# Kernel tuning notes

Measured on AMD Instinct MI355X. Metric: run time of the kernel, lower is better.

The kernel has to match this reference:

```python
import jax, jax.numpy as jnp
import numpy as np

D_MODEL = 1024
D_STATE = 16
EXPAND = 2
D_INNER = EXPAND * D_MODEL
DT_RANK = 64  # ceil(1024/16)
D_CONV = 4


def setup_inputs() -> dict:
    key = jax.random.key(0)
    ks = jax.random.split(key, 8)
    s = 0.02
    x = jax.random.normal(ks[0], (2, 2048, D_MODEL), dtype=jnp.float32)
    W_in = jax.random.normal(ks[1], (D_MODEL, 2 * D_INNER), dtype=jnp.float32) * s
    W_conv = jax.random.normal(ks[2], (D_CONV, D_INNER), dtype=jnp.float32) * s  # depthwise taps
    b_conv = jnp.zeros((D_INNER,), dtype=jnp.float32)
    W_xproj = jax.random.normal(ks[3], (D_INNER, DT_RANK + 2 * D_STATE), dtype=jnp.float32) * s
    W_dt = jax.random.normal(ks[4], (DT_RANK, D_INNER), dtype=jnp.float32) * s
    b_dt = jnp.zeros((D_INNER,), dtype=jnp.float32)
    A_log = jnp.broadcast_to(jnp.log(jnp.arange(1, D_STATE + 1, dtype=jnp.float32)), (D_INNER, D_STATE))
    D = jnp.ones((D_INNER,), dtype=jnp.float32)
    W_out = jax.random.normal(ks[5], (D_INNER, D_MODEL), dtype=jnp.float32) * s
    return {"x": x, "W_in": W_in, "W_conv": W_conv, "b_conv": b_conv,
            "W_xproj": W_xproj, "W_dt": W_dt, "b_dt": b_dt,
            "A_log": A_log, "D": D, "W_out": W_out}


def _silu(v):
    return v * jax.nn.sigmoid(v)


def reference(x, W_in, W_conv, b_conv, W_xproj, W_dt, b_dt, A_log, D, W_out):
    B_, L, _ = x.shape
    xz = x @ W_in                     # [B, L, 2*d_inner]
    x_in, z = jnp.split(xz, 2, axis=-1)
    # causal depthwise conv1d (torch padding=d_conv-1 then slice to seq_len)
    pad = D_CONV - 1
    x_pad = jnp.pad(x_in, ((0, 0), (pad, 0), (0, 0)))
    x_conv = b_conv
    x_conv = sum(x_pad[:, k:k + L, :] * W_conv[k] for k in range(D_CONV)) + b_conv
    x_in = _silu(x_conv)              # [B, L, d_inner]
    dbc = x_in @ W_xproj
    dt = jax.nn.softplus(dbc[..., :DT_RANK] @ W_dt + b_dt)   # [B, L, d_inner]
    Bm = dbc[..., DT_RANK:DT_RANK + D_STATE]                  # [B, L, d_state]
    Cm = dbc[..., DT_RANK + D_STATE:]                          # [B, L, d_state]
    A = -jnp.exp(A_log)                                        # [d_inner, d_state]

    def step(state, inp):
        x_t, dt_t, B_t, C_t = inp   # [B,d_inner], [B,d_inner], [B,d_state], [B,d_state]
        dA = jnp.exp(jnp.clip(dt_t[:, :, None] * A[None], -10.0, 10.0))
        dB = dt_t[:, :, None] * B_t[:, None, :]
        state = jnp.clip(state * dA + x_t[:, :, None] * dB, -10.0, 10.0)
        y_t = jnp.einsum('bdn,bn->bd', state, C_t) + D * x_t
        return state, y_t

    tm = lambda a: jnp.swapaxes(a, 0, 1)  # time-major
    state0 = jnp.zeros((B_, D_INNER, D_STATE), dtype=x.dtype)
    _, ys = jax.lax.scan(step, state0, (tm(x_in), tm(dt), tm(Bm), tm(Cm)))
    y = jnp.swapaxes(ys, 0, 1)            # [B, L, d_inner]
    y = y * _silu(z)
    return y @ W_out                       # [B, L, d_model]
```

## Files before the change

### kernel.cpp

```cpp
#include <hip/hip_runtime.h>
#include <math.h>

#define D_MODEL 1024
#define D_INNER 2048
#define D_STATE 16
#define DT_RANK 64
#define LSEQ 2048
#define NBATCH 2
#define M_TOT (NBATCH * LSEQ)
#define DBC_STRIDE 128
#define CH 64
#define NCH (LSEQ / CH)
#define KSPL 8
#define OKSPL 2

typedef unsigned short ushort_t;
typedef unsigned int uint_t;
typedef __attribute__((ext_vector_type(8))) short bf16x8;
typedef __attribute__((ext_vector_type(4))) float f32x4;

__device__ __forceinline__ ushort_t f2bf_rne(float f) {
    uint_t u = __float_as_uint(f);
    u += 0x7fffu + ((u >> 16) & 1u);
    return (ushort_t)(u >> 16);
}
__device__ __forceinline__ float bf2f(ushort_t h) {
    return __uint_as_float(((uint_t)h) << 16);
}
__device__ __forceinline__ float fexp2(float x) {
#if __has_builtin(__builtin_amdgcn_exp2f)
    return __builtin_amdgcn_exp2f(x);
#else
    return exp2f(x);
#endif
}
__device__ __forceinline__ float frcp(float x) {
#if __has_builtin(__builtin_amdgcn_rcpf)
    return __builtin_amdgcn_rcpf(x);
#else
    return 1.f / x;
#endif
}
__device__ __forceinline__ float clip10(float x) {
#if __has_builtin(__builtin_amdgcn_fmed3f)
    return __builtin_amdgcn_fmed3f(x, -10.f, 10.f);
#else
    return fminf(fmaxf(x, -10.f), 10.f);
#endif
}

#define LOG2E 1.44269504f
#define NLOG2E10 -14.4269504f

#define BAR()   __builtin_amdgcn_s_barrier()
#define LGKM0() asm volatile("s_waitcnt lgkmcnt(0)" ::: "memory")
#define GLDS(SRC, DST)                                                         \
    __builtin_amdgcn_global_load_lds(                                          \
        (const __attribute__((address_space(1))) void*)(SRC),                  \
        (__attribute__((address_space(3))) void*)(DST), 16, 0, 0)

#define LDFRAG_B(SRC)                                                          \
    _Pragma("unroll")                                                          \
    for (int nf = 0; nf < 4; ++nf)                                             \
        fB[nf] = *reinterpret_cast<const bf16x8*>(                             \
            &(SRC)[(bRow + nf * 16 + fm) * 32 + swz * 8]);

#define LDFRAG_A(SRC, MOFF)                                                    \
    _Pragma("unroll")                                                          \
    for (int mf = 0; mf < 4; ++mf)                                             \
        fA[mf] = *reinterpret_cast<const bf16x8*>(                             \
            &(SRC)[(aRow + (MOFF + mf) * 16 + fm) * 32 + swz * 8]);

#define MFMA_QUAD(MOFF)                                                        \
    __builtin_amdgcn_s_setprio(1);                                             \
    _Pragma("unroll")                                                          \
    for (int mf = 0; mf < 4; ++mf)                                             \
        _Pragma("unroll")                                                      \
        for (int nf = 0; nf < 4; ++nf)                                         \
            acc[MOFF + mf][nf] = __builtin_amdgcn_mfma_f32_16x16x32_bf16(      \
                fA[mf], fB[nf], acc[MOFF + mf][nf], 0, 0, 0);                  \
    __builtin_amdgcn_s_setprio(0);

#define KIN 1024
#define KTI (KIN / 64)

__global__ __launch_bounds__(512, 2) void gemm256_inproj(
    const ushort_t* __restrict__ Ah, const ushort_t* __restrict__ BTh,
    float* __restrict__ C, float* __restrict__ AUX)
{
    __shared__ __align__(1024) ushort_t smem[65536];
    const int tid  = threadIdx.x;
    const int lane = tid & 63;
    const int w    = tid >> 6;
    const int wm   = w >> 2;
    const int wn   = w & 3;
    const int fm   = lane & 15, fk = lane >> 4;
    const int swz  = fk ^ ((fm >> 1) & 3);
    const int aRow = wm * 128;
    const int bRow = wn * 64;
    const int m0   = blockIdx.y * 256;
    const int n0   = blockIdx.x * 256;
    const int rbase = w * 16 + (lane >> 2);
    const int ssw   = ((lane & 3) ^ ((lane >> 3) & 3)) * 8;

    f32x4 acc[8][4] = {};

    auto stage = [&](const ushort_t* __restrict__ g, int grow0, int kcol,
                     int regUS) {
        #pragma unroll
        for (int q = 0; q < 2; ++q) {
            const ushort_t* src =
                g + (size_t)(grow0 + q * 128 + rbase) * KIN + kcol + ssw;
            GLDS(src, smem + regUS + q * 4096 + w * 512);
        }
    };

    stage(Ah,  m0, 0,  0);
    stage(BTh, n0, 0,  32768);
    stage(Ah,  m0, 32, 8192);
    stage(BTh, n0, 32, 32768 + 8192);
    stage(Ah,  m0, 64, 16384);
    stage(BTh, n0, 64, 32768 + 16384);
    asm volatile("s_waitcnt vmcnt(8)" ::: "memory");
    BAR();

    bf16x8 fA[4], fB[4];

    for (int t = 0; t < KTI - 1; ++t) {
        const int bf = t & 1, bn = bf ^ 1;
        const ushort_t* A0 = smem + (bf * 2 + 0) * 8192;
        const ushort_t* A1 = smem + (bf * 2 + 1) * 8192;
        const ushort_t* B0 = smem + 32768 + (bf * 2 + 0) * 8192;
        const ushort_t* B1 = smem + 32768 + (bf * 2 + 1) * 8192;
        const int kc1 = (t + 1) * 64, kc2 = (t + 2) * 64;
        const bool st2 = (t + 2 < KTI);

        LDFRAG_B(B0);
        LDFRAG_A(A0, 0);
        stage(Ah, m0, kc1 + 32, (bn * 2 + 1) * 8192);
        BAR(); LGKM0();
        MFMA_QUAD(0);
        BAR();

        LDFRAG_A(A0, 4);
        stage(BTh, n0, kc1 + 32, 32768 + (bn * 2 + 1) * 8192);
        BAR(); LGKM0();
        MFMA_QUAD(4);
        asm volatile("s_waitcnt vmcnt(8)" ::: "memory");
        BAR();
        __builtin_amdgcn_sched_barrier(0);

        LDFRAG_B(B1);
        LDFRAG_A(A1, 0);
        if (st2) stage(Ah, m0, kc2, (bf * 2 + 0) * 8192);
        BAR(); LGKM0();
        MFMA_QUAD(0);
        BAR();

        LDFRAG_A(A1, 4);
        if (st2) stage(BTh, n0, kc2, 32768 + (bf * 2 + 0) * 8192);
        BAR(); LGKM0();
        MFMA_QUAD(4);
        if (t == KTI - 2) { asm volatile("s_waitcnt vmcnt(4)" ::: "memory"); }
        else              { asm volatile("s_waitcnt vmcnt(6)" ::: "memory"); }
        BAR();
        __builtin_amdgcn_sched_barrier(0);
    }

    {
        const int bf = (KTI - 1) & 1;
        const ushort_t* A0 = smem + (bf * 2 + 0) * 8192;
        const ushort_t* A1 = smem + (bf * 2 + 1) * 8192;
        const ushort_t* B0 = smem + 32768 + (bf * 2 + 0) * 8192;
        const ushort_t* B1 = smem + 32768 + (bf * 2 + 1) * 8192;

        LDFRAG_B(B0);
        LDFRAG_A(A0, 0);
        BAR(); LGKM0();
        MFMA_QUAD(0);
        BAR();

        LDFRAG_A(A0, 4);
        BAR(); LGKM0();
        MFMA_QUAD(4);
        asm volatile("s_waitcnt vmcnt(0)" ::: "memory");
        BAR();

        LDFRAG_B(B1);
        LDFRAG_A(A1, 0);
        BAR(); LGKM0();
        MFMA_QUAD(0);
        BAR();

        LDFRAG_A(A1, 4);
        BAR(); LGKM0();
        MFMA_QUAD(4);
    }

    float* dst = (n0 < D_INNER) ? C : AUX;
    const int csub = (n0 < D_INNER) ? 0 : D_INNER;
    #pragma unroll
    for (int mf = 0; mf < 8; ++mf) {
        int row0 = m0 + aRow + mf * 16 + fk * 4;
        #pragma unroll
        for (int nf = 0; nf < 4; ++nf) {
            int col = n0 + bRow + nf * 16 + fm - csub;
            #pragma unroll
            for (int r = 0; r < 4; ++r)
                dst[(size_t)(row0 + r) * D_INNER + col] = acc[mf][nf][r];
        }
    }
}

#define KOUT 2048
#define NTOUT 16

__global__ __launch_bounds__(512, 2) void gemm256_outproj(
    const ushort_t* __restrict__ Ah, const ushort_t* __restrict__ BTh,
    const ushort_t* __restrict__ BTl, float* __restrict__ P)
{
    __shared__ __align__(1024) ushort_t smem[65536];
    const int tid  = threadIdx.x;
    const int lane = tid & 63;
    const int w    = tid >> 6;
    const int wm   = w & 3;
    const int wn   = w >> 2;
    const int fm   = lane & 15, fk = lane >> 4;
    const int swz  = fk ^ ((fm >> 1) & 3);
    const int aRow = wm * 64;
    const int bRow = wn * 64;
    const int ks   = blockIdx.x >> 3;
    const int n0   = (blockIdx.x & 7) * 128;
    const int m0   = blockIdx.y * 256;
    const int kb   = ks * (KOUT / OKSPL);
    const int rbase = w * 16 + (lane >> 2);
    const int ssw   = ((lane & 3) ^ ((lane >> 3) & 3)) * 8;

    f32x4 acc[4][4] = {};

    auto stageA = [&](int t, int kh) {
        const int kcol = kb + t * 64 + kh * 32;
        const int reg = ((t & 1) * 2 + kh) * 8192;
        #pragma unroll
        for (int q = 0; q < 2; ++q) {
            const ushort_t* src =
                Ah + (size_t)(m0 + q * 128 + rbase) * KOUT + kcol + ssw;
            GLDS(src, smem + reg + q * 4096 + w * 512);
        }
    };
    auto stageB = [&](const ushort_t* __restrict__ B, int base, int t, int kh) {
        const int kcol = kb + t * 64 + kh * 32;
        const int reg = base + ((t & 1) * 2 + kh) * 4096;
        const ushort_t* src = B + (size_t)(n0 + rbase) * KOUT + kcol + ssw;
        GLDS(src, smem + reg + w * 512);
    };

    stageA(0, 0);
    stageA(0, 1);
    stageB(BTh, 32768, 0, 0);
    stageB(BTh, 32768, 0, 1);
    stageB(BTl, 49152, 0, 0);
    stageB(BTl, 49152, 0, 1);
    asm volatile("s_waitcnt vmcnt(3)" ::: "memory");
    BAR();

    bf16x8 fA[4], fB[4];

    for (int t = 0; t < NTOUT - 1; ++t) {
        const int bf = t & 1;
        const ushort_t* A0  = smem + (bf * 2 + 0) * 8192;
        const ushort_t* A1  = smem + (bf * 2 + 1) * 8192;
        const ushort_t* Bh0 = smem + 32768 + (bf * 2 + 0) * 4096;
        const ushort_t* Bh1 = smem + 32768 + (bf * 2 + 1) * 4096;
        const ushort_t* Bl0 = smem + 49152 + (bf * 2 + 0) * 4096;
        const ushort_t* Bl1 = smem + 49152 + (bf * 2 + 1) * 4096;

        LDFRAG_B(Bh0);
        LDFRAG_A(A0, 0);
        stageA(t + 1, 0);
        BAR(); LGKM0();
        MFMA_QUAD(0);
        asm volatile("s_waitcnt vmcnt(3)" ::: "memory");
        BAR();
        __builtin_amdgcn_sched_barrier(0);

        LDFRAG_B(Bl0);
        stageA(t + 1, 1);
        BAR(); LGKM0();
        MFMA_QUAD(0);
        BAR();

        LDFRAG_B(Bh1);
        LDFRAG_A(A1, 0);
        stageB(BTh, 32768, t + 1, 0);
        stageB(BTh, 32768, t + 1, 1);
        BAR(); LGKM0();
        MFMA_QUAD(0);
        asm volatile("s_waitcnt vmcnt(6)" ::: "memory");
        BAR();
        __builtin_amdgcn_sched_barrier(0);

        LDFRAG_B(Bl1);
        stageB(BTl, 49152, t + 1, 0);
        stageB(BTl, 49152, t + 1, 1);
        BAR(); LGKM0();
        MFMA_QUAD(0);
        asm volatile("s_waitcnt vmcnt(3)" ::: "memory");
        BAR();
        __builtin_amdgcn_sched_barrier(0);
    }

    {
        const int bf = (NTOUT - 1) & 1;
        const ushort_t* A0  = smem + (bf * 2 + 0) * 8192;
        const ushort_t* A1  = smem + (bf * 2 + 1) * 8192;
        const ushort_t* Bh0 = smem + 32768 + (bf * 2 + 0) * 4096;
        const ushort_t* Bh1 = smem + 32768 + (bf * 2 + 1) * 4096;
        const ushort_t* Bl0 = smem + 49152 + (bf * 2 + 0) * 4096;
        const ushort_t* Bl1 = smem + 49152 + (bf * 2 + 1) * 4096;

        LDFRAG_B(Bh0);
        LDFRAG_A(A0, 0);
        BAR(); LGKM0();
        MFMA_QUAD(0);
        asm volatile("s_waitcnt vmcnt(1)" ::: "memory");
        BAR();

        LDFRAG_B(Bl0);
        BAR(); LGKM0();
        MFMA_QUAD(0);
        BAR();

        LDFRAG_B(Bh1);
        LDFRAG_A(A1, 0);
        BAR(); LGKM0();
        MFMA_QUAD(0);
        asm volatile("s_waitcnt vmcnt(0)" ::: "memory");
        BAR();

        LDFRAG_B(Bl1);
        BAR(); LGKM0();
        MFMA_QUAD(0);
    }

    float* Pq = P + (size_t)ks * M_TOT * D_MODEL;
    #pragma unroll
    for (int mf = 0; mf < 4; ++mf) {
        int row0 = m0 + aRow + mf * 16 + fk * 4;
        #pragma unroll
        for (int nf = 0; nf < 4; ++nf) {
            int col = n0 + bRow + nf * 16 + fm;
            #pragma unroll
            for (int r = 0; r < 4; ++r)
                Pq[(size_t)(row0 + r) * D_MODEL + col] = acc[mf][nf][r];
        }
    }
}

template <int MODE, int TERMS>
__global__ __launch_bounds__(256) void gemm_bf16s(
    const ushort_t* __restrict__ Ah, const ushort_t* __restrict__ Al,
    const ushort_t* __restrict__ BTh, const ushort_t* __restrict__ BTl,
    float* __restrict__ C, float* __restrict__ AUX, int M, int N, int K)
{
    __shared__ __align__(16) ushort_t smem[4 * 128 * 32];
    ushort_t* sAh = smem;
    ushort_t* sAl = smem + 4096;
    ushort_t* sBh = smem + 8192;
    ushort_t* sBl = smem + 12288;
    const int tid = threadIdx.x;
    const int lane = tid & 63;
    const int m0 = blockIdx.y * 128;
    int ks = 0, nblk = blockIdx.x;
    if (MODE == 3) { ks = blockIdx.x; nblk = 0; }
    const int n0 = nblk * 128;
    const int wave = tid >> 6;
    const int mw = (wave & 1) * 64, nw = (wave >> 1) * 64;
    const int fm = lane & 15, fk = lane >> 4;
    const int swz = fk ^ ((fm >> 1) & 3);

    f32x4 acc[4][4] = {};

    const int r_st0 = tid >> 2, cp0 = tid & 3;
    const int r_st1 = (256 + tid) >> 2, cp1 = tid & 3;
    const int cl0 = cp0 ^ ((r_st0 >> 1) & 3);
    const int cl1 = cp1 ^ ((r_st1 >> 1) & 3);
    const int ldsb0 = (tid & ~63) * 16;
    const int ldsb1 = (256 + (tid & ~63)) * 16;

    const int kbeg = (MODE == 3) ? ks * (K / KSPL) : 0;
    const int kend = (MODE == 3) ? kbeg + K / KSPL : K;

    for (int k0 = kbeg; k0 < kend; k0 += 32) {
        __syncthreads();
        {
            size_t ga0 = (size_t)(m0 + r_st0) * K + k0 + cl0 * 8;
            size_t ga1 = (size_t)(m0 + r_st1) * K + k0 + cl1 * 8;
            size_t gb0 = (size_t)(n0 + r_st0) * K + k0 + cl0 * 8;
            size_t gb1 = (size_t)(n0 + r_st1) * K + k0 + cl1 * 8;
            GLDS(Ah + ga0, (char*)sAh + ldsb0);
            GLDS(Ah + ga1, (char*)sAh + ldsb1);
            if (TERMS >= 3) {
                GLDS(Al + ga0, (char*)sAl + ldsb0);
                GLDS(Al + ga1, (char*)sAl + ldsb1);
            }
            GLDS(BTh + gb0, (char*)sBh + ldsb0);
            GLDS(BTh + gb1, (char*)sBh + ldsb1);
            if (TERMS >= 2) {
                GLDS(BTl + gb0, (char*)sBl + ldsb0);
                GLDS(BTl + gb1, (char*)sBl + ldsb1);
            }
        }
        __syncthreads();

        bf16x8 fAh[4], fAl[4], fBh[4], fBl[4];
        #pragma unroll
        for (int t = 0; t < 4; ++t) {
            int ra = (mw + t * 16 + fm) * 32 + swz * 8;
            int rb = (nw + t * 16 + fm) * 32 + swz * 8;
            fAh[t] = *reinterpret_cast<const bf16x8*>(&sAh[ra]);
            if (TERMS >= 3) fAl[t] = *reinterpret_cast<const bf16x8*>(&sAl[ra]);
            fBh[t] = *reinterpret_cast<const bf16x8*>(&sBh[rb]);
            if (TERMS >= 2) fBl[t] = *reinterpret_cast<const bf16x8*>(&sBl[rb]);
        }
        #pragma unroll
        for (int i = 0; i < 4; ++i)
            #pragma unroll
            for (int j = 0; j < 4; ++j) {
                acc[i][j] = __builtin_amdgcn_mfma_f32_16x16x32_bf16(fAh[i], fBh[j], acc[i][j], 0, 0, 0);
                if (TERMS >= 3)
                    acc[i][j] = __builtin_amdgcn_mfma_f32_16x16x32_bf16(fAl[i], fBh[j], acc[i][j], 0, 0, 0);
                if (TERMS >= 2)
                    acc[i][j] = __builtin_amdgcn_mfma_f32_16x16x32_bf16(fAh[i], fBl[j], acc[i][j], 0, 0, 0);
            }
    }

    float* Cq = (MODE == 3) ? C + (size_t)ks * M * N : C;
    #pragma unroll
    for (int i = 0; i < 4; ++i) {
        int row0 = m0 + mw + i * 16 + fk * 4;
        #pragma unroll
        for (int j = 0; j < 4; ++j) {
            int col = n0 + nw + j * 16 + fm;
            if (MODE == 5) {
                const float* bias = (const float*)AUX;
                float bc_ = bias[col];
                #pragma unroll
                for (int r = 0; r < 4; ++r) {
                    float t = acc[i][j][r] + bc_;
                    C[(size_t)(row0 + r) * N + col] =
                        fmaxf(t, 0.f) + log1pf(__expf(-fabsf(t)));
                }
            } else {
                #pragma unroll
                for (int r = 0; r < 4; ++r)
                    Cq[(size_t)(row0 + r) * N + col] = acc[i][j][r];
            }
        }
    }
}

__global__ __launch_bounds__(256) void xproj_red_k(
    const float* __restrict__ dbcp, float* __restrict__ dbc,
    ushort_t* __restrict__ dbch)
{
    int g = blockIdx.x * 256 + threadIdx.x;
    int m = g >> 7, c = g & 127;
    float s = 0.f;
    #pragma unroll
    for (int ks = 0; ks < KSPL; ++ks)
        s += dbcp[(size_t)ks * M_TOT * DBC_STRIDE + g];
    dbc[g] = s;
    if (c < 64)
        dbch[(size_t)m * 64 + c] = f2bf_rne(s);
}

__global__ __launch_bounds__(256) void outred_k(
    const float* __restrict__ p, float* __restrict__ out)
{
    int i4 = (blockIdx.x * 256 + threadIdx.x) * 4;
    f32x4 a = *reinterpret_cast<const f32x4*>(p + i4);
    f32x4 b = *reinterpret_cast<const f32x4*>(p + (size_t)M_TOT * D_MODEL + i4);
    *reinterpret_cast<f32x4*>(out + i4) = a + b;
}

__global__ __launch_bounds__(256) void cast_h_k(
    const float* __restrict__ X, ushort_t* __restrict__ Xh)
{
    int i4 = (blockIdx.x * 256 + threadIdx.x) * 4;
    float4 v = *reinterpret_cast<const float4*>(X + i4);
    ushort2 a = make_ushort2(f2bf_rne(v.x), f2bf_rne(v.y));
    ushort2 b = make_ushort2(f2bf_rne(v.z), f2bf_rne(v.w));
    *reinterpret_cast<ushort2*>(Xh + i4)     = a;
    *reinterpret_cast<ushort2*>(Xh + i4 + 2) = b;
}

__global__ __launch_bounds__(256) void transpose_cast_k(
    const float* __restrict__ W, ushort_t* __restrict__ Th, ushort_t* __restrict__ Tl,
    int K, int N)
{
    __shared__ float tile[32][33];
    int n0 = blockIdx.x * 32, k0 = blockIdx.y * 32;
    int tx = threadIdx.x & 31, ty = threadIdx.x >> 5;
    #pragma unroll
    for (int i = 0; i < 32; i += 8)
        tile[ty + i][tx] = W[(size_t)(k0 + ty + i) * N + n0 + tx];
    __syncthreads();
    #pragma unroll
    for (int i = 0; i < 32; i += 8) {
        float v = tile[tx][ty + i];
        ushort_t h = f2bf_rne(v);
        ushort_t l = f2bf_rne(v - bf2f(h));
        size_t o = (size_t)(n0 + ty + i) * K + k0 + tx;
        Th[o] = h; Tl[o] = l;
    }
}

__global__ __launch_bounds__(256) void transpose_cast_pad_k(
    const float* __restrict__ W, ushort_t* __restrict__ Th, int K, int N)
{
    __shared__ float tile[32][33];
    int n0 = blockIdx.x * 32, k0 = blockIdx.y * 32;
    int tx = threadIdx.x & 31, ty = threadIdx.x >> 5;
    #pragma unroll
    for (int i = 0; i < 32; i += 8)
        tile[ty + i][tx] = (n0 + tx < N) ? W[(size_t)(k0 + ty + i) * N + n0 + tx] : 0.f;
    __syncthreads();
    #pragma unroll
    for (int i = 0; i < 32; i += 8) {
        float v = tile[tx][ty + i];
        size_t o = (size_t)(n0 + ty + i) * K + k0 + tx;
        Th[o] = f2bf_rne(v);
    }
}

__global__ __launch_bounds__(256) void conv_silu_k(
    const float* __restrict__ xbuf, const float* __restrict__ Wc,
    const float* __restrict__ bc, ushort_t* __restrict__ xinh,
    float* __restrict__ xf)
{
    __shared__ float tile[67][64];
    const int c0 = blockIdx.x * 64;
    const int m0 = blockIdx.y * 64;
    const int bstart = m0 & ~(LSEQ - 1);
    const int tid = threadIdx.x;

    for (int e = tid; e < 67 * 64; e += 256) {
        int r = e >> 6, c = e & 63;
        int g = m0 - 3 + r;
        tile[r][c] = (g >= bstart) ? xbuf[(size_t)g * D_INNER + c0 + c] : 0.f;
    }
    __syncthreads();

    const int c_l = tid & 63, mg = tid >> 6;
    const int c = c0 + c_l;
    const float w0 = Wc[c], w1 = Wc[D_INNER + c];
    const float w2 = Wc[2 * D_INNER + c], w3 = Wc[3 * D_INNER + c];
    const float bb = bc[c];
    #pragma unroll
    for (int mi = 0; mi < 16; ++mi) {
        int r = mg * 16 + mi;
        float acc = bb + tile[r][c_l] * w0 + tile[r + 1][c_l] * w1
                       + tile[r + 2][c_l] * w2 + tile[r + 3][c_l] * w3;
        float sv = acc / (1.f + __expf(-acc));
        xinh[(size_t)(m0 + r) * D_INNER + c] = f2bf_rne(sv);
        xf[(size_t)(m0 + r) * D_INNER + c] = sv;
    }
}

__global__ __launch_bounds__(256) void scan_sum_k4(
    const float* __restrict__ dtf, const float* __restrict__ xf,
    const float* __restrict__ dbc, const float* __restrict__ A_log,
    float* __restrict__ asumb, float* __restrict__ sendb)
{
    __shared__ float sdt[2][8][256];
    __shared__ float sx[2][8][256];
    __shared__ float sB[64][16];
    const int tid = threadIdx.x;
    const int lane = tid & 63;
    const int w = tid >> 6;
    const int c0 = blockIdx.x << 8;
    const int ck = blockIdx.y;
    const int b  = blockIdx.z;
    const size_t mbase = (size_t)b * LSEQ + (size_t)ck * CH;
    const int d = c0 + tid;

    auto stageG = [&](int G, int bf) {
        #pragma unroll
        for (int p = 0; p < 2; ++p) {
            const int r = w + p * 4;
            const size_t g = (mbase + G * 8 + r) * D_INNER + c0 + lane * 4;
            GLDS(dtf + g, &sdt[bf][r][0]);
            GLDS(xf + g,  &sx[bf][r][0]);
        }
    };

    {
        const int rbc = w * 16 + (lane >> 2);
        GLDS(dbc + (mbase + rbc) * DBC_STRIDE + 64 + (lane & 3) * 4,
             &sB[w * 16][0]);
    }
    stageG(0, 0);
    stageG(1, 1);

    float AdnL2[16];
    #pragma unroll
    for (int n = 0; n < 16; ++n)
        AdnL2[n] = -__expf(A_log[d * D_STATE + n]) * LOG2E;

    float s[16] = {};
    float asum[16] = {};

    asm volatile("s_waitcnt vmcnt(4)" ::: "memory");
    BAR();

    for (int G = 0; G < 8; ++G) {
        const int bf = G & 1;
        #pragma unroll
        for (int t = 0; t < 8; ++t) {
            const int rr = G * 8 + t;
            const float dv = sdt[bf][t][tid];
            const float xv = sx[bf][t][tid];
            const float p  = dv * xv;
            #pragma unroll
            for (int n = 0; n < 16; ++n) {
                float a = fmaxf(dv * AdnL2[n], NLOG2E10);
                asum[n] += a;
                float e = fexp2(a);
                s[n] = clip10(fmaf(s[n], e, p * sB[rr][n]));
            }
        }
        BAR();
        if (G + 2 < 8) {
            stageG(G + 2, bf);
            asm volatile("s_waitcnt vmcnt(4)" ::: "memory");
        } else if (G == 6) {
            asm volatile("s_waitcnt vmcnt(0)" ::: "memory");
        }
        BAR();
        __builtin_amdgcn_sched_barrier(0);
    }

    #pragma unroll
    for (int n = 0; n < 16; ++n) {
        size_t o = (((size_t)(b * NCH + ck) * 16) + n) * D_INNER + d;
        asumb[o] = asum[n];
        sendb[o] = s[n];
    }
}

__global__ __launch_bounds__(256) void scan_fix_k2(
    const float* __restrict__ asumb, const float* __restrict__ sendb,
    float* __restrict__ sinb)
{
    int g = blockIdx.x * 256 + threadIdx.x;
    int d = g & (D_INNER - 1);
    int n = (g >> 11) & 15;
    int b = g >> 15;
    float s = 0.f;
    for (int ck = 0; ck < NCH; ++ck) {
        size_t idx = (((size_t)(b * NCH + ck) * 16) + n) * D_INNER + d;
        sinb[idx] = s;
        s = clip10(fmaf(s, fexp2(asumb[idx]), sendb[idx]));
    }
}

__global__ __launch_bounds__(256) void scan_apply_k4(
    const float* __restrict__ dtf, const float* __restrict__ xf,
    const float* __restrict__ dbc, const float* __restrict__ zf,
    const float* __restrict__ sinb, const float* __restrict__ A_log,
    const float* __restrict__ Dv, ushort_t* __restrict__ Yh)
{
    __shared__ float sdt[2][8][256];
    __shared__ float sx[2][8][256];
    __shared__ float sz[2][8][256];
    __shared__ float sBC[64][32];
    const int tid = threadIdx.x;
    const int lane = tid & 63;
    const int w = tid >> 6;
    const int c0 = blockIdx.x << 8;
    const int ck = blockIdx.y;
    const int b  = blockIdx.z;
    const size_t mbase = (size_t)b * LSEQ + (size_t)ck * CH;
    const int d = c0 + tid;

    auto stageG = [&](int G, int bf) {
        #pragma unroll
        for (int p = 0; p < 2; ++p) {
            const int r = w + p * 4;
            const size_t g = (mbase + G * 8 + r) * D_INNER + c0 + lane * 4;
            GLDS(dtf + g, &sdt[bf][r][0]);
            GLDS(xf + g,  &sx[bf][r][0]);
            GLDS(zf + g,  &sz[bf][r][0]);
        }
    };

    #pragma unroll
    for (int p = 0; p < 2; ++p) {
        const int rbc = w * 16 + p * 8 + (lane >> 3);
        GLDS(dbc + (mbase + rbc) * DBC_STRIDE + 64 + (lane & 7) * 4,
             &sBC[w * 16 + p * 8][0]);
    }
    stageG(0, 0);
    stageG(1, 1);

    float AdnL2[16];
    #pragma unroll
    for (int n = 0; n < 16; ++n)
        AdnL2[n] = -__expf(A_log[d * D_STATE + n]) * LOG2E;
    const float Dd = Dv[d];

    float s[16];
    #pragma unroll
    for (int n = 0; n < 16; ++n)
        s[n] = sinb[(((size_t)(b * NCH + ck) * 16) + n) * D_INNER + d];

    asm volatile("s_waitcnt vmcnt(6)" ::: "memory");
    BAR();

    for (int G = 0; G < 8; ++G) {
        const int bf = G & 1;
        #pragma unroll
        for (int t = 0; t < 8; ++t) {
            const int rr = G * 8 + t;
            const float dv = sdt[bf][t][tid];
            const float xv = sx[bf][t][tid];
            const float p  = dv * xv;
            float y0 = Dd * xv, y1 = 0.f, y2 = 0.f, y3 = 0.f;
            #pragma unroll
            for (int n = 0; n < 16; n += 4) {
                float a0 = fmaxf(dv * AdnL2[n + 0], NLOG2E10);
                float a1 = fmaxf(dv * AdnL2[n + 1], NLOG2E10);
                float a2 = fmaxf(dv * AdnL2[n + 2], NLOG2E10);
                float a3 = fmaxf(dv * AdnL2[n + 3], NLOG2E10);
                s[n + 0] = clip10(fmaf(s[n + 0], fexp2(a0), p * sBC[rr][n + 0]));
                s[n + 1] = clip10(fmaf(s[n + 1], fexp2(a1), p * sBC[rr][n + 1]));
                s[n + 2] = clip10(fmaf(s[n + 2], fexp2(a2), p * sBC[rr][n + 2]));
                s[n + 3] = clip10(fmaf(s[n + 3], fexp2(a3), p * sBC[rr][n + 3]));
                y0 = fmaf(s[n + 0], sBC[rr][16 + n + 0], y0);
                y1 = fmaf(s[n + 1], sBC[rr][16 + n + 1], y1);
                y2 = fmaf(s[n + 2], sBC[rr][16 + n + 2], y2);
                y3 = fmaf(s[n + 3], sBC[rr][16 + n + 3], y3);
            }
            const float y = (y0 + y1) + (y2 + y3);
            const float zz = sz[bf][t][tid];
            const float gate = zz * frcp(1.f + fexp2(zz * -LOG2E));
            Yh[(mbase + rr) * D_INNER + d] = f2bf_rne(y * gate);
        }
        BAR();
        if (G + 2 < 8) {
            stageG(G + 2, bf);
            asm volatile("s_waitcnt vmcnt(6)" ::: "memory");
        } else if (G == 6) {
            asm volatile("s_waitcnt vmcnt(0)" ::: "memory");
        }
        BAR();
        __builtin_amdgcn_sched_barrier(0);
    }
}

extern "C" void kernel_launch(void* const* d_in, const int* in_sizes, int n_in,
                              void* d_out, int out_size, void* d_ws, size_t ws_size,
                              hipStream_t stream)
{
    const float* x       = (const float*)d_in[0];
    const float* W_in    = (const float*)d_in[1];
    const float* W_conv  = (const float*)d_in[2];
    const float* b_conv  = (const float*)d_in[3];
    const float* W_xproj = (const float*)d_in[4];
    const float* W_dt    = (const float*)d_in[5];
    const float* b_dt    = (const float*)d_in[6];
    const float* A_log   = (const float*)d_in[7];
    const float* Dv      = (const float*)d_in[8];
    const float* W_out   = (const float*)d_in[9];
    float* out = (float*)d_out;

    float* xbuf = (float*)d_ws;
    float* zf   = xbuf + (size_t)M_TOT * D_INNER;
    float* dbc  = zf + (size_t)M_TOT * D_INNER;
    float* BCT  = dbc + (size_t)M_TOT * DBC_STRIDE;
    ushort_t* xh     = (ushort_t*)(BCT + (size_t)32 * M_TOT);
    ushort_t* xl     = xh + (size_t)M_TOT * D_MODEL;
    ushort_t* WinTh  = xl + (size_t)M_TOT * D_MODEL;
    ushort_t* WinTl  = WinTh + (size_t)2 * D_INNER * D_MODEL;
    ushort_t* WoutTh = WinTl + (size_t)2 * D_INNER * D_MODEL;
    ushort_t* WoutTl = WoutTh + (size_t)D_MODEL * D_INNER;
    ushort_t* WxTh   = WoutTl + (size_t)D_MODEL * D_INNER;
    ushort_t* WxTl   = WxTh + (size_t)DBC_STRIDE * D_INNER;
    ushort_t* xinh   = WxTl + (size_t)DBC_STRIDE * D_INNER;
    ushort_t* xinl   = xinh + (size_t)M_TOT * D_INNER;
    ushort_t* yh     = xinl + (size_t)M_TOT * D_INNER;
    ushort_t* yl     = yh + (size_t)M_TOT * D_INNER;
    ushort_t* WdtTh  = yl + (size_t)M_TOT * D_INNER;
    ushort_t* dbch   = WdtTh + (size_t)D_INNER * DT_RANK;
    float* xf   = (float*)xh;
    float* dtf  = (float*)xinh;
    float* dbcp = (float*)yh;
    float* pout = (float*)xh;
    const size_t NSUM = (size_t)NBATCH * NCH * D_INNER * D_STATE;
    float* asumb = xbuf;
    float* sendb = xbuf + NSUM;
    float* sinb  = xbuf + 2 * NSUM;

    cast_h_k<<<(M_TOT * D_MODEL) / 1024, 256, 0, stream>>>(x, xh);
    transpose_cast_pad_k<<<dim3((2 * D_INNER) / 32, D_MODEL / 32), 256, 0, stream>>>(
        W_in, WinTh, D_MODEL, 2 * D_INNER);
    transpose_cast_k<<<dim3(D_MODEL / 32, D_INNER / 32), 256, 0, stream>>>(
        W_out, WoutTh, WoutTl, D_INNER, D_MODEL);
    transpose_cast_pad_k<<<dim3(DBC_STRIDE / 32, D_INNER / 32), 256, 0, stream>>>(
        W_xproj, WxTh, D_INNER, DT_RANK + 2 * D_STATE);
    transpose_cast_pad_k<<<dim3(D_INNER / 32, DT_RANK / 32), 256, 0, stream>>>(
        W_dt, WdtTh, DT_RANK, D_INNER);

    gemm256_inproj<<<dim3(16, 16), 512, 0, stream>>>(xh, WinTh, xbuf, zf);
    conv_silu_k<<<dim3(D_INNER / 64, M_TOT / 64), 256, 0, stream>>>(
        xbuf, W_conv, b_conv, xinh, xf);
    gemm_bf16s<3, 1><<<dim3(KSPL, 32), 256, 0, stream>>>(
        xinh, nullptr, WxTh, nullptr, dbcp, nullptr, M_TOT, DBC_STRIDE, D_INNER);
    xproj_red_k<<<(M_TOT * DBC_STRIDE) / 256, 256, 0, stream>>>(dbcp, dbc, dbch);
    gemm_bf16s<5, 1><<<dim3(D_INNER / 128, M_TOT / 128), 256, 0, stream>>>(
        dbch, nullptr, WdtTh, nullptr, dtf, (float*)b_dt, M_TOT, D_INNER, DT_RANK);
    scan_sum_k4<<<dim3(D_INNER / 256, NCH, NBATCH), 256, 0, stream>>>(
        dtf, xf, dbc, A_log, asumb, sendb);
    scan_fix_k2<<<(NBATCH * D_STATE * D_INNER) / 256, 256, 0, stream>>>(
        asumb, sendb, sinb);
    scan_apply_k4<<<dim3(D_INNER / 256, NCH, NBATCH), 256, 0, stream>>>(
        dtf, xf, dbc, zf, sinb, A_log, Dv, yh);
    gemm256_outproj<<<dim3(16, 16), 512, 0, stream>>>(yh, WoutTh, WoutTl, pout);
    outred_k<<<(M_TOT * D_MODEL) / 1024, 256, 0, stream>>>(pout, out);
}
```

Measured before the change: 335.4 us.

## Split scan state dimension across two half-wave lanes per channel

The chunked scan kernels now use 512 threads per block, and each channel's 16 state elements are split across two lanes that own 8 states each. The apply kernel combines the partial y dot products with a cross-half-wave shuffle, and only the lower half does the gate and the store. This halves per-thread register state and serial work per thread, raising parallelism and occupancy for the latency-bound recurrence. The cost is redundant dt/x shared-memory reads, duplicated exp work per row, a shuffle per timestep, and half the lanes idle during the output writes.

```diff
diff --git a/kernel.cpp b/kernel.cpp
--- a/kernel.cpp
+++ b/kernel.cpp
@@ -568,50 +568,47 @@
     }
 }
 
-__global__ __launch_bounds__(256) void scan_sum_k4(
+__global__ __launch_bounds__(512) void scan_sum_k5(
     const float* __restrict__ dtf, const float* __restrict__ xf,
     const float* __restrict__ dbc, const float* __restrict__ A_log,
     float* __restrict__ asumb, float* __restrict__ sendb)
 {
     __shared__ float sdt[2][8][256];
     __shared__ float sx[2][8][256];
-    __shared__ float sB[64][16];
+    __shared__ float sBC[64][32];
     const int tid = threadIdx.x;
     const int lane = tid & 63;
     const int w = tid >> 6;
+    const int dloc = (w << 5) + (lane & 31);
+    const int n0 = (lane >> 5) * 8;
     const int c0 = blockIdx.x << 8;
     const int ck = blockIdx.y;
     const int b  = blockIdx.z;
     const size_t mbase = (size_t)b * LSEQ + (size_t)ck * CH;
-    const int d = c0 + tid;
+    const int d = c0 + dloc;
 
     auto stageG = [&](int G, int bf) {
-        #pragma unroll
-        for (int p = 0; p < 2; ++p) {
-            const int r = w + p * 4;
-            const size_t g = (mbase + G * 8 + r) * D_INNER + c0 + lane * 4;
-            GLDS(dtf + g, &sdt[bf][r][0]);
-            GLDS(xf + g,  &sx[bf][r][0]);
-        }
+        const size_t g = (mbase + G * 8 + w) * D_INNER + c0 + lane * 4;
+        GLDS(dtf + g, &sdt[bf][w][0]);
+        GLDS(xf + g,  &sx[bf][w][0]);
     };
 
     {
-        const int rbc = w * 16 + (lane >> 2);
-        GLDS(dbc + (mbase + rbc) * DBC_STRIDE + 64 + (lane & 3) * 4,
-             &sB[w * 16][0]);
+        const int row = tid >> 3, col = (tid & 7) * 4;
+        GLDS(dbc + (mbase + row) * DBC_STRIDE + 64 + col, &sBC[w * 8][0]);
     }
     stageG(0, 0);
     stageG(1, 1);
 
-    float AdnL2[16];
-    #pragma unroll
-    for (int n = 0; n < 16; ++n)
-        AdnL2[n] = -__expf(A_log[d * D_STATE + n]) * LOG2E;
-
-    float s[16] = {};
-    float asum[16] = {};
-
-    asm volatile("s_waitcnt vmcnt(4)" ::: "memory");
+    float AdnL2[8];
+    #pragma unroll
+    for (int j = 0; j < 8; ++j)
+        AdnL2[j] = -__expf(A_log[d * D_STATE + n0 + j]) * LOG2E;
+
+    float s[8] = {};
+    float asum[8] = {};
+
+    asm volatile("s_waitcnt vmcnt(2)" ::: "memory");
     BAR();
 
     for (int G = 0; G < 8; ++G) {
@@ -619,21 +616,21 @@
         #pragma unroll
         for (int t = 0; t < 8; ++t) {
             const int rr = G * 8 + t;
-            const float dv = sdt[bf][t][tid];
-            const float xv = sx[bf][t][tid];
+            const float dv = sdt[bf][t][dloc];
+            const float xv = sx[bf][t][dloc];
             const float p  = dv * xv;
             #pragma unroll
-            for (int n = 0; n < 16; ++n) {
-                float a = fmaxf(dv * AdnL2[n], NLOG2E10);
-                asum[n] += a;
+            for (int j = 0; j < 8; ++j) {
+                float a = fmaxf(dv * AdnL2[j], NLOG2E10);
+                asum[j] += a;
                 float e = fexp2(a);
-                s[n] = clip10(fmaf(s[n], e, p * sB[rr][n]));
+                s[j] = clip10(fmaf(s[j], e, p * sBC[rr][n0 + j]));
             }
         }
         BAR();
         if (G + 2 < 8) {
             stageG(G + 2, bf);
-            asm volatile("s_waitcnt vmcnt(4)" ::: "memory");
+            asm volatile("s_waitcnt vmcnt(2)" ::: "memory");
         } else if (G == 6) {
             asm volatile("s_waitcnt vmcnt(0)" ::: "memory");
         }
@@ -642,10 +639,10 @@
     }
 
     #pragma unroll
-    for (int n = 0; n < 16; ++n) {
-        size_t o = (((size_t)(b * NCH + ck) * 16) + n) * D_INNER + d;
-        asumb[o] = asum[n];
-        sendb[o] = s[n];
+    for (int j = 0; j < 8; ++j) {
+        size_t o = (((size_t)(b * NCH + ck) * 16) + n0 + j) * D_INNER + d;
+        asumb[o] = asum[j];
+        sendb[o] = s[j];
     }
 }
 
@@ -665,7 +662,7 @@
     }
 }
 
-__global__ __launch_bounds__(256) void scan_apply_k4(
+__global__ __launch_bounds__(512) void scan_apply_k5(
     const float* __restrict__ dtf, const float* __restrict__ xf,
     const float* __restrict__ dbc, const float* __restrict__ zf,
     const float* __restrict__ sinb, const float* __restrict__ A_log,
@@ -678,44 +675,40 @@
     const int tid = threadIdx.x;
     const int lane = tid & 63;
     const int w = tid >> 6;
+    const int dloc = (w << 5) + (lane & 31);
+    const int n0 = (lane >> 5) * 8;
     const int c0 = blockIdx.x << 8;
     const int ck = blockIdx.y;
     const int b  = blockIdx.z;
     const size_t mbase = (size_t)b * LSEQ + (size_t)ck * CH;
-    const int d = c0 + tid;
+    const int d = c0 + dloc;
 
     auto stageG = [&](int G, int bf) {
-        #pragma unroll
-        for (int p = 0; p < 2; ++p) {
-            const int r = w + p * 4;
-            const size_t g = (mbase + G * 8 + r) * D_INNER + c0 + lane * 4;
-            GLDS(dtf + g, &sdt[bf][r][0]);
-            GLDS(xf + g,  &sx[bf][r][0]);
-            GLDS(zf + g,  &sz[bf][r][0]);
-        }
+        const size_t g = (mbase + G * 8 + w) * D_INNER + c0 + lane * 4;
+        GLDS(dtf + g, &sdt[bf][w][0]);
+        GLDS(xf + g,  &sx[bf][w][0]);
+        GLDS(zf + g,  &sz[bf][w][0]);
     };
 
-    #pragma unroll
-    for (int p = 0; p < 2; ++p) {
-        const int rbc = w * 16 + p * 8 + (lane >> 3);
-        GLDS(dbc + (mbase + rbc) * DBC_STRIDE + 64 + (lane & 7) * 4,
-             &sBC[w * 16 + p * 8][0]);
+    {
+        const int row = tid >> 3, col = (tid & 7) * 4;
+        GLDS(dbc + (mbase + row) * DBC_STRIDE + 64 + col, &sBC[w * 8][0]);
     }
     stageG(0, 0);
     stageG(1, 1);
 
-    float AdnL2[16];
-    #pragma unroll
-    for (int n = 0; n < 16; ++n)
-        AdnL2[n] = -__expf(A_log[d * D_STATE + n]) * LOG2E;
+    float AdnL2[8];
+    #pragma unroll
+    for (int j = 0; j < 8; ++j)
+        AdnL2[j] = -__expf(A_log[d * D_STATE + n0 + j]) * LOG2E;
     const float Dd = Dv[d];
 
-    float s[16];
-    #pragma unroll
-    for (int n = 0; n < 16; ++n)
-        s[n] = sinb[(((size_t)(b * NCH + ck) * 16) + n) * D_INNER + d];
-
-    asm volatile("s_waitcnt vmcnt(6)" ::: "memory");
+    float s[8];
+    #pragma unroll
+    for (int j = 0; j < 8; ++j)
+        s[j] = sinb[(((size_t)(b * NCH + ck) * 16) + n0 + j) * D_INNER + d];
+
+    asm volatile("s_waitcnt vmcnt(3)" ::: "memory");
     BAR();
 
     for (int G = 0; G < 8; ++G) {
@@ -723,34 +716,32 @@
         #pragma unroll
         for (int t = 0; t < 8; ++t) {
             const int rr = G * 8 + t;
-            const float dv = sdt[bf][t][tid];
-            const float xv = sx[bf][t][tid];
+            const float dv = sdt[bf][t][dloc];
+            const float xv = sx[bf][t][dloc];
             const float p  = dv * xv;
-            float y0 = Dd * xv, y1 = 0.f, y2 = 0.f, y3 = 0.f;
+            float y0 = 0.f, y1 = 0.f;
             #pragma unroll
-            for (int n = 0; n < 16; n += 4) {
-                float a0 = fmaxf(dv * AdnL2[n + 0], NLOG2E10);
-                float a1 = fmaxf(dv * AdnL2[n + 1], NLOG2E10);
-                float a2 = fmaxf(dv * AdnL2[n + 2], NLOG2E10);
-                float a3 = fmaxf(dv * AdnL2[n + 3], NLOG2E10);
-                s[n + 0] = clip10(fmaf(s[n + 0], fexp2(a0), p * sBC[rr][n + 0]));
-                s[n + 1] = clip10(fmaf(s[n + 1], fexp2(a1), p * sBC[rr][n + 1]));
-                s[n + 2] = clip10(fmaf(s[n + 2], fexp2(a2), p * sBC[rr][n + 2]));
-                s[n + 3] = clip10(fmaf(s[n + 3], fexp2(a3), p * sBC[rr][n + 3]));
-                y0 = fmaf(s[n + 0], sBC[rr][16 + n + 0], y0);
-                y1 = fmaf(s[n + 1], sBC[rr][16 + n + 1], y1);
-                y2 = fmaf(s[n + 2], sBC[rr][16 + n + 2], y2);
-                y3 = fmaf(s[n + 3], sBC[rr][16 + n + 3], y3);
+            for (int j = 0; j < 8; j += 2) {
+                float a0 = fmaxf(dv * AdnL2[j + 0], NLOG2E10);
+                float a1 = fmaxf(dv * AdnL2[j + 1], NLOG2E10);
+                s[j + 0] = clip10(fmaf(s[j + 0], fexp2(a0), p * sBC[rr][n0 + j + 0]));
+                s[j + 1] = clip10(fmaf(s[j + 1], fexp2(a1), p * sBC[rr][n0 + j + 1]));
+                y0 = fmaf(s[j + 0], sBC[rr][16 + n0 + j + 0], y0);
+                y1 = fmaf(s[j + 1], sBC[rr][16 + n0 + j + 1], y1);
             }
-            const float y = (y0 + y1) + (y2 + y3);
-            const float zz = sz[bf][t][tid];
-            const float gate = zz * frcp(1.f + fexp2(zz * -LOG2E));
-            Yh[(mbase + rr) * D_INNER + d] = f2bf_rne(y * gate);
+            float y = y0 + y1;
+            y += __shfl_xor(y, 32, 64);
+            if (lane < 32) {
+                const float yf = y + Dd * xv;
+                const float zz = sz[bf][t][dloc];
+                const float gate = zz * frcp(1.f + fexp2(zz * -LOG2E));
+                Yh[(mbase + rr) * D_INNER + d] = f2bf_rne(yf * gate);
+            }
         }
         BAR();
         if (G + 2 < 8) {
             stageG(G + 2, bf);
-            asm volatile("s_waitcnt vmcnt(6)" ::: "memory");
+            asm volatile("s_waitcnt vmcnt(3)" ::: "memory");
         } else if (G == 6) {
             asm volatile("s_waitcnt vmcnt(0)" ::: "memory");
         }
@@ -820,11 +811,11 @@
     xproj_red_k<<<(M_TOT * DBC_STRIDE) / 256, 256, 0, stream>>>(dbcp, dbc, dbch);
     gemm_bf16s<5, 1><<<dim3(D_INNER / 128, M_TOT / 128), 256, 0, stream>>>(
         dbch, nullptr, WdtTh, nullptr, dtf, (float*)b_dt, M_TOT, D_INNER, DT_RANK);
-    scan_sum_k4<<<dim3(D_INNER / 256, NCH, NBATCH), 256, 0, stream>>>(
+    scan_sum_k5<<<dim3(D_INNER / 256, NCH, NBATCH), 512, 0, stream>>>(
         dtf, xf, dbc, A_log, asumb, sendb);
     scan_fix_k2<<<(NBATCH * D_STATE * D_INNER) / 256, 256, 0, stream>>>(
         asumb, sendb, sinb);
-    scan_apply_k4<<<dim3(D_INNER / 256, NCH, NBATCH), 256, 0, stream>>>(
+    scan_apply_k5<<<dim3(D_INNER / 256, NCH, NBATCH), 512, 0, stream>>>(
         dtf, xf, dbc, zf, sinb, A_log, Dv, yh);
     gemm256_outproj<<<dim3(16, 16), 512, 0, stream>>>(yh, WoutTh, WoutTl, pout);
     outred_k<<<(M_TOT * D_MODEL) / 1024, 256, 0, stream>>>(pout, out);
```

After: 339.3 us (median of 2 runs). No clear change (+1.2%).
